# Performance work log

Hardware: AMD Instinct MI355X
Metric: run time of the kernel (lower is better)

Reference implementation:

```python
import jax, jax.numpy as jnp
import numpy as np

NUM_LEVELS = 16
LEVEL_DIM = 2
BASE_RES = 16
LOG2_HASH = 24
DESIRED_RES = 2048
D = 2
PRIMES = (1, 2654435761)
N_POINTS = 2097152
HIDDEN = 64
OUT_DIM = 3
LC_INIT = 1e-4


def _level_meta():
    # torch-ngp gridencoder level geometry (align_corners=False)
    S = np.log2(DESIRED_RES / BASE_RES) / (NUM_LEVELS - 1)
    max_params = 2 ** LOG2_HASH
    scales, res, offsets = [], [], [0]
    for l in range(NUM_LEVELS):
        s = 2.0 ** (l * S) * BASE_RES - 1.0
        r = int(np.ceil(s)) + 1
        p = min(max_params, (r + 1) ** D)
        p = int(np.ceil(p / 8) * 8)  # align to 8
        scales.append(s)
        res.append(r)
        offsets.append(offsets[-1] + p)
    return scales, res, offsets

SCALES, RES, OFFSETS = _level_meta()
TOTAL_PARAMS = OFFSETS[-1]  # 8827256 for this config


def hashgrid_encode(x01, embeddings):
    # x01: [N, 2] in [0,1]; embeddings: [TOTAL_PARAMS, LEVEL_DIM]
    feats = []
    for l in range(NUM_LEVELS):
        scale, r = SCALES[l], RES[l]
        size = OFFSETS[l + 1] - OFFSETS[l]
        dense = (r + 1) ** D <= size  # all levels dense for 2D / log2=24
        pos = x01 * jnp.float32(scale) + 0.5
        pg = jnp.floor(pos)
        frac = pos - pg  # [N,2] bilinear weights
        pgi = pg.astype(jnp.uint32)
        acc = jnp.zeros((x01.shape[0], LEVEL_DIM), x01.dtype)
        for cx in (0, 1):
            for cy in (0, 1):
                gx = pgi[:, 0] + jnp.uint32(cx)
                gy = pgi[:, 1] + jnp.uint32(cy)
                if dense:
                    idx = gx + gy * jnp.uint32(r + 1)
                else:
                    idx = (gx * jnp.uint32(PRIMES[0])) ^ (gy * jnp.uint32(PRIMES[1]))
                idx = (idx % jnp.uint32(size)).astype(jnp.int32) + OFFSETS[l]
                wx = frac[:, 0] if cx else 1.0 - frac[:, 0]
                wy = frac[:, 1] if cy else 1.0 - frac[:, 1]
                acc = acc + (wx * wy)[:, None] * embeddings[idx]
        feats.append(acc)
    return jnp.concatenate(feats, axis=-1)  # [N, 32]


def setup_inputs():
    key = jax.random.key(0)
    ks = jax.random.split(key, 5)
    in_feat = NUM_LEVELS * LEVEL_DIM  # 32

    def lin(k, fan_in, fan_out):
        b = 1.0 / np.sqrt(fan_in)
        kw, kb = jax.random.split(k)
        w = jax.random.uniform(kw, (fan_out, fan_in), jnp.float32, -b, b)
        bb = jax.random.uniform(kb, (fan_out,), jnp.float32, -b, b)
        return w, bb

    w0, b0 = lin(ks[1], in_feat, HIDDEN)
    w1, b1 = lin(ks[2], HIDDEN, HIDDEN)
    w2, b2 = lin(ks[3], HIDDEN, OUT_DIM)
    return {
        "x": jax.random.uniform(ks[0], (N_POINTS, 2), jnp.float32),
        "cmax": jnp.ones((2,), jnp.float32),
        "embeddings": jax.random.uniform(ks[4], (TOTAL_PARAMS, LEVEL_DIM), jnp.float32, -LC_INIT, LC_INIT),
        "w0": w0, "b0": b0, "w1": w1, "b1": b1, "w2": w2, "b2": b2,
    }


def reference(x, cmax, embeddings, w0, b0, w1, b1, w2, b2):
    x01 = x / cmax[::-1][None]  # cmax.flip(-1)
    out_lc0 = hashgrid_encode(x01, embeddings)
    h = jax.nn.relu(out_lc0)            # lc_act='relu'
    h = jax.nn.relu(h @ w0.T + b0)      # layer 0
    h = jax.nn.relu(h @ w1.T + b1)      # layer 1
    h = h @ w2.T + b2                   # layer 2 (no act)
    return h, out_lc0
```

## Files before the change

kernel.cpp:

```cpp
#include <hip/hip_runtime.h>
#include <math.h>

#define NLEV 16
#define RES  256
#define NBIN 65536

typedef _Float16 f16;
typedef f16 f16x8 __attribute__((ext_vector_type(8)));
typedef float f32x4 __attribute__((ext_vector_type(4)));

struct LevelMeta {
    float scale[NLEV];
    int   r1[NLEV];
    int   off[NLEV];
};

struct alignas(8) F4 { float x, y, z, w; };

__device__ inline unsigned spread2d(unsigned v) {
    v = (v | (v << 4)) & 0x0F0Fu;
    v = (v | (v << 2)) & 0x3333u;
    v = (v | (v << 1)) & 0x5555u;
    return v;
}

__device__ inline unsigned bin_of(float x0, float x1) {
    int bx = (int)(x0 * (float)RES); bx = bx < 0 ? 0 : (bx > RES - 1 ? RES - 1 : bx);
    int by = (int)(x1 * (float)RES); by = by < 0 ? 0 : (by > RES - 1 ? RES - 1 : by);
    return spread2d((unsigned)bx) | (spread2d((unsigned)by) << 1);
}

__global__ __launch_bounds__(256)
void zero_kernel(unsigned* __restrict__ hist) {
    ((uint4*)hist)[blockIdx.x * 256 + threadIdx.x] = uint4{0, 0, 0, 0};
}

__global__ __launch_bounds__(256)
void hist_kernel(const float* __restrict__ x, const float* __restrict__ cmax,
                 unsigned* __restrict__ hist, unsigned short* __restrict__ bin16,
                 unsigned* __restrict__ seq) {
    int p = blockIdx.x * 256 + threadIdx.x;
    float2 xy = ((const float2*)x)[p];
    unsigned b = bin_of(xy.x / cmax[1], xy.y / cmax[0]);
    unsigned s = atomicAdd(&hist[b], 1u);
    bin16[p] = (unsigned short)b;
    seq[p] = s;
}

__global__ __launch_bounds__(256)
void scanA_kernel(const unsigned* __restrict__ hist, unsigned* __restrict__ sums) {
    __shared__ unsigned ws[4];
    int t = threadIdx.x;
    unsigned s = hist[blockIdx.x * 256 + t];
#pragma unroll
    for (int o = 1; o < 64; o <<= 1) s += (unsigned)__shfl_xor((int)s, o);
    if ((t & 63) == 0) ws[t >> 6] = s;
    __syncthreads();
    if (t == 0) sums[blockIdx.x] = ws[0] + ws[1] + ws[2] + ws[3];
}

__global__ __launch_bounds__(256)
void scanB_kernel(unsigned* __restrict__ sums) {
    __shared__ unsigned ws[4];
    int t = threadIdx.x, lane = t & 63, w = t >> 6;
    unsigned v = sums[t];
    unsigned xs = v;
#pragma unroll
    for (int o = 1; o < 64; o <<= 1) {
        unsigned y = (unsigned)__shfl_up((int)xs, o);
        if (lane >= o) xs += y;
    }
    if (lane == 63) ws[w] = xs;
    __syncthreads();
    unsigned wo = 0;
    for (int k = 0; k < w; ++k) wo += ws[k];
    sums[t] = wo + xs - v;
}

__global__ __launch_bounds__(256)
void scanC_kernel(const unsigned* __restrict__ hist, const unsigned* __restrict__ sums,
                  unsigned* __restrict__ base) {
    __shared__ unsigned ws[4];
    int t = threadIdx.x, lane = t & 63, w = t >> 6;
    int gb = blockIdx.x * 256 + t;
    unsigned v = hist[gb];
    unsigned xs = v;
#pragma unroll
    for (int o = 1; o < 64; o <<= 1) {
        unsigned y = (unsigned)__shfl_up((int)xs, o);
        if (lane >= o) xs += y;
    }
    if (lane == 63) ws[w] = xs;
    __syncthreads();
    unsigned wo = 0;
    for (int k = 0; k < w; ++k) wo += ws[k];
    base[gb] = sums[blockIdx.x] + wo + xs - v;
}

__global__ __launch_bounds__(256)
void scatter_kernel(const float* __restrict__ x, const float* __restrict__ cmax,
                    const unsigned short* __restrict__ bin16,
                    const unsigned* __restrict__ seq,
                    const unsigned* __restrict__ base,
                    unsigned* __restrict__ pidx, float2* __restrict__ px) {
    int p = blockIdx.x * 256 + threadIdx.x;
    unsigned b = bin16[p];
    unsigned rank = base[b] + seq[p];
    pidx[rank] = (unsigned)p;
    float2 xy = ((const float2*)x)[p];
    float2 v; v.x = xy.x / cmax[1]; v.y = xy.y / cmax[0];
    px[rank] = v;
}

__global__ __launch_bounds__(256, 4)
void hashmlp_kernel(const float* __restrict__ x,
                    const float* __restrict__ cmax,
                    const unsigned* __restrict__ pidx,
                    const float2* __restrict__ px,
                    const float* __restrict__ emb,
                    const float* __restrict__ w0,
                    const float* __restrict__ b0,
                    const float* __restrict__ w1,
                    const float* __restrict__ b1,
                    const float* __restrict__ w2,
                    const float* __restrict__ b2,
                    float* __restrict__ out,
                    int npts, int nblk,
                    LevelMeta meta)
{
    __shared__ f16 wbuf[4][4608];

    const int tid  = threadIdx.x;
    const int lane = tid & 63;
    const int wave = tid >> 6;

    int bid = blockIdx.x;
    int cpx = nblk >> 3;
    int swz = (bid & 7) * cpx + (bid >> 3);
    const int g = swz * 256 + tid;
    const int gblk = swz * 256 + wave * 64;

    int p;
    float x0, x1;
    if (pidx) {
        p = (int)pidx[g];
        float2 xy = px[g];
        x0 = xy.x; x1 = xy.y;
    } else {
        p = g;
        float2 xy = ((const float2*)x)[p];
        x0 = xy.x / cmax[1];
        x1 = xy.y / cmax[0];
    }

    float fr[32];
#pragma unroll
    for (int hh = 0; hh < 2; ++hh) {
        F4 lo[8], hi[8];
#pragma unroll
        for (int i = 0; i < 8; ++i) {
            const int l = hh * 8 + i;
            float p0 = x0 * meta.scale[l] + 0.5f;
            float p1 = x1 * meta.scale[l] + 0.5f;
            int i0 = (int)floorf(p0);
            int i1 = (int)floorf(p1);
            const float* ebf = emb + 2 * (meta.off[l] + i1 * meta.r1[l] + i0);
            lo[i] = *(const F4*)ebf;
            hi[i] = *(const F4*)(ebf + 2 * meta.r1[l]);
        }
        __builtin_amdgcn_sched_barrier(0);
#pragma unroll
        for (int i = 0; i < 8; ++i) {
            const int l = hh * 8 + i;
            float p0 = x0 * meta.scale[l] + 0.5f;
            float p1 = x1 * meta.scale[l] + 0.5f;
            float g0 = floorf(p0), g1 = floorf(p1);
            float f0 = p0 - g0, f1 = p1 - g1;
            float omf0 = 1.f - f0, omf1 = 1.f - f1;
            float w00 = omf0 * omf1, w01 = omf0 * f1, w10 = f0 * omf1, w11 = f0 * f1;
            float a0 = w00 * lo[i].x; a0 += w01 * hi[i].x; a0 += w10 * lo[i].z; a0 += w11 * hi[i].z;
            float a1 = w00 * lo[i].y; a1 += w01 * hi[i].y; a1 += w10 * lo[i].w; a1 += w11 * hi[i].w;
            fr[2 * l]     = a0;
            fr[2 * l + 1] = a1;
        }
    }

    float* outlc = out + (size_t)npts * 3 + (size_t)p * 32;
#pragma unroll
    for (int c = 0; c < 8; ++c) {
        float4 v;
        v.x = fr[4 * c]; v.y = fr[4 * c + 1]; v.z = fr[4 * c + 2]; v.w = fr[4 * c + 3];
        ((float4*)outlc)[c] = v;
    }

    f16* fbuf = wbuf[wave];
#pragma unroll
    for (int c = 0; c < 4; ++c) {
        f16x8 v;
#pragma unroll
        for (int j = 0; j < 8; ++j)
            v[j] = (f16)(fmaxf(fr[8 * c + j], 0.f) * 16384.f);
        *(f16x8*)&fbuf[lane * 40 + c * 8] = v;
    }

    const int lr = lane & 15;
    const int lg = lane >> 4;
    f16* hbuf = wbuf[wave];

    {
        f16x8 bf[4];
        float bia[4];
#pragma unroll
        for (int nt = 0; nt < 4; ++nt) {
            const float* wr = w0 + (nt * 16 + lr) * 32 + lg * 8;
            float4 wa = ((const float4*)wr)[0];
            float4 wb = ((const float4*)wr)[1];
            f16x8 v;
            v[0] = (f16)wa.x; v[1] = (f16)wa.y; v[2] = (f16)wa.z; v[3] = (f16)wa.w;
            v[4] = (f16)wb.x; v[5] = (f16)wb.y; v[6] = (f16)wb.z; v[7] = (f16)wb.w;
            bf[nt] = v;
            bia[nt] = b0[nt * 16 + lr];
        }
#pragma unroll
        for (int mt = 3; mt >= 0; --mt) {
            f16x8 a = *(const f16x8*)&fbuf[(mt * 16 + lr) * 40 + lg * 8];
            __builtin_amdgcn_s_setprio(1);
            f32x4 c[4];
#pragma unroll
            for (int nt = 0; nt < 4; ++nt) {
                f32x4 z = {0.f, 0.f, 0.f, 0.f};
                c[nt] = __builtin_amdgcn_mfma_f32_16x16x32_f16(a, bf[nt], z, 0, 0, 0);
            }
            __builtin_amdgcn_s_setprio(0);
#pragma unroll
            for (int nt = 0; nt < 4; ++nt)
#pragma unroll
                for (int q = 0; q < 4; ++q) {
                    float h = fmaxf(c[nt][q] * (1.0f / 16384.f) + bia[nt], 0.f);
                    hbuf[(mt * 16 + lg * 4 + q) * 72 + nt * 16 + lr] = (f16)h;
                }
        }
    }

    {
        f16x8 bf[4][2];
        float bia[4];
#pragma unroll
        for (int nt = 0; nt < 4; ++nt) {
            const float* wr = w1 + (nt * 16 + lr) * 64;
#pragma unroll
            for (int h = 0; h < 2; ++h) {
                float4 wa = ((const float4*)(wr + 32 * h + lg * 8))[0];
                float4 wb = ((const float4*)(wr + 32 * h + lg * 8))[1];
                f16x8 v;
                v[0] = (f16)wa.x; v[1] = (f16)wa.y; v[2] = (f16)wa.z; v[3] = (f16)wa.w;
                v[4] = (f16)wb.x; v[5] = (f16)wb.y; v[6] = (f16)wb.z; v[7] = (f16)wb.w;
                bf[nt][h] = v;
            }
            bia[nt] = b1[nt * 16 + lr];
        }
#pragma unroll
        for (int mt = 0; mt < 4; ++mt) {
            f16x8 a0 = *(const f16x8*)&hbuf[(mt * 16 + lr) * 72 + lg * 8];
            f16x8 a1 = *(const f16x8*)&hbuf[(mt * 16 + lr) * 72 + 32 + lg * 8];
            __builtin_amdgcn_s_setprio(1);
            f32x4 c[4];
#pragma unroll
            for (int nt = 0; nt < 4; ++nt) {
                f32x4 z = {0.f, 0.f, 0.f, 0.f};
                z = __builtin_amdgcn_mfma_f32_16x16x32_f16(a0, bf[nt][0], z, 0, 0, 0);
                c[nt] = __builtin_amdgcn_mfma_f32_16x16x32_f16(a1, bf[nt][1], z, 0, 0, 0);
            }
            __builtin_amdgcn_s_setprio(0);
#pragma unroll
            for (int nt = 0; nt < 4; ++nt)
#pragma unroll
                for (int q = 0; q < 4; ++q) {
                    float h = fmaxf(c[nt][q] + bia[nt], 0.f);
                    hbuf[(mt * 16 + lg * 4 + q) * 72 + nt * 16 + lr] = (f16)h;
                }
        }
    }

    {
        f16x8 bf0 = {};
        f16x8 bf1 = {};
        float bia2 = 0.f;
        if (lr < 3) {
            const float* wr = w2 + lr * 64;
#pragma unroll
            for (int h = 0; h < 2; ++h) {
                float4 wa = ((const float4*)(wr + 32 * h + lg * 8))[0];
                float4 wb = ((const float4*)(wr + 32 * h + lg * 8))[1];
                f16x8 v;
                v[0] = (f16)wa.x; v[1] = (f16)wa.y; v[2] = (f16)wa.z; v[3] = (f16)wa.w;
                v[4] = (f16)wb.x; v[5] = (f16)wb.y; v[6] = (f16)wb.z; v[7] = (f16)wb.w;
                if (h) bf1 = v; else bf0 = v;
            }
            bia2 = b2[lr];
        }
#pragma unroll
        for (int mt = 0; mt < 4; ++mt) {
            f16x8 a0 = *(const f16x8*)&hbuf[(mt * 16 + lr) * 72 + lg * 8];
            f16x8 a1 = *(const f16x8*)&hbuf[(mt * 16 + lr) * 72 + 32 + lg * 8];
            __builtin_amdgcn_s_setprio(1);
            f32x4 c = {0.f, 0.f, 0.f, 0.f};
            c = __builtin_amdgcn_mfma_f32_16x16x32_f16(a0, bf0, c, 0, 0, 0);
            c = __builtin_amdgcn_mfma_f32_16x16x32_f16(a1, bf1, c, 0, 0, 0);
            __builtin_amdgcn_s_setprio(0);
            if (lr < 3) {
#pragma unroll
                for (int q = 0; q < 4; ++q) {
                    int row = mt * 16 + lg * 4 + q;
                    int po = pidx ? (int)pidx[gblk + row] : (gblk + row);
                    out[(size_t)po * 3 + lr] = c[q] + bia2;
                }
            }
        }
    }
}

extern "C" void kernel_launch(void* const* d_in, const int* in_sizes, int n_in,
                              void* d_out, int out_size, void* d_ws, size_t ws_size,
                              hipStream_t stream) {
    const float* x    = (const float*)d_in[0];
    const float* cmax = (const float*)d_in[1];
    const float* emb  = (const float*)d_in[2];
    const float* w0   = (const float*)d_in[3];
    const float* b0   = (const float*)d_in[4];
    const float* w1   = (const float*)d_in[5];
    const float* b1   = (const float*)d_in[6];
    const float* w2   = (const float*)d_in[7];
    const float* b2   = (const float*)d_in[8];
    const int npts = in_sizes[0] / 2;
    const int nblk = npts / 256;

    LevelMeta meta;
    const double S = log2(2048.0 / 16.0) / 15.0;
    long long off = 0;
    for (int l = 0; l < NLEV; ++l) {
        double s = pow(2.0, l * S) * 16.0 - 1.0;
        int r = (int)ceil(s) + 1;
        long long pc = (long long)(r + 1) * (r + 1);
        if (pc > (1ll << 24)) pc = (1ll << 24);
        pc = ((pc + 7) / 8) * 8;
        meta.scale[l] = (float)s;
        meta.r1[l]    = r + 1;
        meta.off[l]   = (int)off;
        off += pc;
    }

    size_t need = (size_t)NBIN * 8 + 256 * 4 + (size_t)npts * 18;
    if (ws_size >= need && (npts & 255) == 0 && (nblk & 7) == 0) {
        unsigned* hist = (unsigned*)d_ws;
        unsigned* base = hist + NBIN;
        unsigned* sums = base + NBIN;
        unsigned* pidx = sums + 256;
        unsigned* seq  = pidx + npts;
        float2*   px   = (float2*)(seq + npts);
        unsigned short* bin16 = (unsigned short*)(px + npts);

        hipLaunchKernelGGL(zero_kernel, dim3(NBIN / 1024), dim3(256), 0, stream, hist);
        hipLaunchKernelGGL(hist_kernel, dim3(nblk), dim3(256), 0, stream, x, cmax, hist, bin16, seq);
        hipLaunchKernelGGL(scanA_kernel, dim3(NBIN / 256), dim3(256), 0, stream, hist, sums);
        hipLaunchKernelGGL(scanB_kernel, dim3(1), dim3(256), 0, stream, sums);
        hipLaunchKernelGGL(scanC_kernel, dim3(NBIN / 256), dim3(256), 0, stream, hist, sums, base);
        hipLaunchKernelGGL(scatter_kernel, dim3(nblk), dim3(256), 0, stream, x, cmax, bin16, seq, base, pidx, px);
        hipLaunchKernelGGL(hashmlp_kernel, dim3(nblk), dim3(256), 0, stream,
                           x, cmax, pidx, px, emb, w0, b0, w1, b1, w2, b2,
                           (float*)d_out, npts, nblk, meta);
    } else {
        hipLaunchKernelGGL(hashmlp_kernel, dim3(nblk), dim3(256), 0, stream,
                           x, cmax, (const unsigned*)nullptr, (const float2*)nullptr,
                           emb, w0, b0, w1, b1, w2, b2,
                           (float*)d_out, npts, nblk, meta);
    }
}
```

Measured before the change: 402.2 us.

## Split fused hash-encode+MLP kernel into separate encode and MLP kernels

The fused kernel is split into an encode kernel that gathers embeddings (using inline-asm dwordx4 loads followed by an explicit vmcnt wait) and writes the 32-float features, and a separate MLP kernel that reads those features back in original point order. The MLP now runs on contiguous points, which removes the pidx indirection and scattered output writes, and each kernel needs fewer registers and less LDS. The cost is an extra launch plus a full re-read of the 256 MB feature buffer from memory.

```diff
diff --git a/kernel.cpp b/kernel.cpp
--- a/kernel.cpp
+++ b/kernel.cpp
@@ -15,7 +15,12 @@
     int   off[NLEV];
 };
 
-struct alignas(8) F4 { float x, y, z, w; };
+__device__ inline f32x4 gload4(const float* p) {
+    f32x4 r;
+    asm volatile("global_load_dwordx4 %0, %1, off"
+                 : "=v"(r) : "v"(p) : "memory");
+    return r;
+}
 
 __device__ inline unsigned spread2d(unsigned v) {
     v = (v | (v << 4)) & 0x0F0Fu;
@@ -113,32 +118,19 @@
 }
 
 __global__ __launch_bounds__(256, 4)
-void hashmlp_kernel(const float* __restrict__ x,
-                    const float* __restrict__ cmax,
-                    const unsigned* __restrict__ pidx,
-                    const float2* __restrict__ px,
-                    const float* __restrict__ emb,
-                    const float* __restrict__ w0,
-                    const float* __restrict__ b0,
-                    const float* __restrict__ w1,
-                    const float* __restrict__ b1,
-                    const float* __restrict__ w2,
-                    const float* __restrict__ b2,
-                    float* __restrict__ out,
-                    int npts, int nblk,
-                    LevelMeta meta)
+void encode_kernel(const float* __restrict__ x,
+                   const float* __restrict__ cmax,
+                   const unsigned* __restrict__ pidx,
+                   const float2* __restrict__ px,
+                   const float* __restrict__ emb,
+                   float* __restrict__ out,
+                   int npts, int nblk,
+                   LevelMeta meta)
 {
-    __shared__ f16 wbuf[4][4608];
-
-    const int tid  = threadIdx.x;
-    const int lane = tid & 63;
-    const int wave = tid >> 6;
-
     int bid = blockIdx.x;
     int cpx = nblk >> 3;
     int swz = (bid & 7) * cpx + (bid >> 3);
-    const int g = swz * 256 + tid;
-    const int gblk = swz * 256 + wave * 64;
+    const int g = swz * 256 + threadIdx.x;
 
     int p;
     float x0, x1;
@@ -153,10 +145,11 @@
         x1 = xy.y / cmax[0];
     }
 
-    float fr[32];
+    float* outlc = out + (size_t)npts * 3 + (size_t)p * 32;
+
 #pragma unroll
     for (int hh = 0; hh < 2; ++hh) {
-        F4 lo[8], hi[8];
+        f32x4 lo[8], hi[8];
 #pragma unroll
         for (int i = 0; i < 8; ++i) {
             const int l = hh * 8 + i;
@@ -165,10 +158,13 @@
             int i0 = (int)floorf(p0);
             int i1 = (int)floorf(p1);
             const float* ebf = emb + 2 * (meta.off[l] + i1 * meta.r1[l] + i0);
-            lo[i] = *(const F4*)ebf;
-            hi[i] = *(const F4*)(ebf + 2 * meta.r1[l]);
-        }
+            lo[i] = gload4(ebf);
+            hi[i] = gload4(ebf + 2 * meta.r1[l]);
+        }
+        asm volatile("s_waitcnt vmcnt(0)" ::: "memory");
         __builtin_amdgcn_sched_barrier(0);
+
+        float fr[16];
 #pragma unroll
         for (int i = 0; i < 8; ++i) {
             const int l = hh * 8 + i;
@@ -178,34 +174,59 @@
             float f0 = p0 - g0, f1 = p1 - g1;
             float omf0 = 1.f - f0, omf1 = 1.f - f1;
             float w00 = omf0 * omf1, w01 = omf0 * f1, w10 = f0 * omf1, w11 = f0 * f1;
-            float a0 = w00 * lo[i].x; a0 += w01 * hi[i].x; a0 += w10 * lo[i].z; a0 += w11 * hi[i].z;
-            float a1 = w00 * lo[i].y; a1 += w01 * hi[i].y; a1 += w10 * lo[i].w; a1 += w11 * hi[i].w;
-            fr[2 * l]     = a0;
-            fr[2 * l + 1] = a1;
-        }
-    }
-
-    float* outlc = out + (size_t)npts * 3 + (size_t)p * 32;
-#pragma unroll
-    for (int c = 0; c < 8; ++c) {
-        float4 v;
-        v.x = fr[4 * c]; v.y = fr[4 * c + 1]; v.z = fr[4 * c + 2]; v.w = fr[4 * c + 3];
-        ((float4*)outlc)[c] = v;
-    }
-
-    f16* fbuf = wbuf[wave];
-#pragma unroll
-    for (int c = 0; c < 4; ++c) {
-        f16x8 v;
-#pragma unroll
-        for (int j = 0; j < 8; ++j)
-            v[j] = (f16)(fmaxf(fr[8 * c + j], 0.f) * 16384.f);
-        *(f16x8*)&fbuf[lane * 40 + c * 8] = v;
-    }
+            float a0 = w00 * lo[i][0]; a0 += w01 * hi[i][0]; a0 += w10 * lo[i][2]; a0 += w11 * hi[i][2];
+            float a1 = w00 * lo[i][1]; a1 += w01 * hi[i][1]; a1 += w10 * lo[i][3]; a1 += w11 * hi[i][3];
+            fr[2 * i]     = a0;
+            fr[2 * i + 1] = a1;
+        }
+#pragma unroll
+        for (int c = 0; c < 4; ++c) {
+            float4 v;
+            v.x = fr[4 * c]; v.y = fr[4 * c + 1]; v.z = fr[4 * c + 2]; v.w = fr[4 * c + 3];
+            ((float4*)outlc)[hh * 4 + c] = v;
+        }
+    }
+}
+
+__global__ __launch_bounds__(256, 4)
+void mlp_kernel(const float* __restrict__ lc,
+                const float* __restrict__ w0,
+                const float* __restrict__ b0,
+                const float* __restrict__ w1,
+                const float* __restrict__ b1,
+                const float* __restrict__ w2,
+                const float* __restrict__ b2,
+                float* __restrict__ out,
+                int npts)
+{
+    __shared__ f16 wbuf[4][4608];
+
+    const int tid  = threadIdx.x;
+    const int lane = tid & 63;
+    const int wave = tid >> 6;
+    const int g0 = blockIdx.x * 256 + wave * 64;
 
     const int lr = lane & 15;
     const int lg = lane >> 4;
     f16* hbuf = wbuf[wave];
+
+    f16x8 afr[4];
+#pragma unroll
+    for (int mt = 0; mt < 4; ++mt) {
+        const float* fp = lc + (size_t)(g0 + mt * 16 + lr) * 32 + lg * 8;
+        float4 fa = ((const float4*)fp)[0];
+        float4 fb = ((const float4*)fp)[1];
+        f16x8 v;
+        v[0] = (f16)(fmaxf(fa.x, 0.f) * 16384.f);
+        v[1] = (f16)(fmaxf(fa.y, 0.f) * 16384.f);
+        v[2] = (f16)(fmaxf(fa.z, 0.f) * 16384.f);
+        v[3] = (f16)(fmaxf(fa.w, 0.f) * 16384.f);
+        v[4] = (f16)(fmaxf(fb.x, 0.f) * 16384.f);
+        v[5] = (f16)(fmaxf(fb.y, 0.f) * 16384.f);
+        v[6] = (f16)(fmaxf(fb.z, 0.f) * 16384.f);
+        v[7] = (f16)(fmaxf(fb.w, 0.f) * 16384.f);
+        afr[mt] = v;
+    }
 
     {
         f16x8 bf[4];
@@ -222,14 +243,13 @@
             bia[nt] = b0[nt * 16 + lr];
         }
 #pragma unroll
-        for (int mt = 3; mt >= 0; --mt) {
-            f16x8 a = *(const f16x8*)&fbuf[(mt * 16 + lr) * 40 + lg * 8];
+        for (int mt = 0; mt < 4; ++mt) {
             __builtin_amdgcn_s_setprio(1);
             f32x4 c[4];
 #pragma unroll
             for (int nt = 0; nt < 4; ++nt) {
                 f32x4 z = {0.f, 0.f, 0.f, 0.f};
-                c[nt] = __builtin_amdgcn_mfma_f32_16x16x32_f16(a, bf[nt], z, 0, 0, 0);
+                c[nt] = __builtin_amdgcn_mfma_f32_16x16x32_f16(afr[mt], bf[nt], z, 0, 0, 0);
             }
             __builtin_amdgcn_s_setprio(0);
 #pragma unroll
@@ -312,8 +332,7 @@
 #pragma unroll
                 for (int q = 0; q < 4; ++q) {
                     int row = mt * 16 + lg * 4 + q;
-                    int po = pidx ? (int)pidx[gblk + row] : (gblk + row);
-                    out[(size_t)po * 3 + lr] = c[q] + bia2;
+                    out[(size_t)(g0 + row) * 3 + lr] = c[q] + bia2;
                 }
             }
         }
@@ -350,6 +369,9 @@
         off += pc;
     }
 
+    float* outp = (float*)d_out;
+    const float* lc = outp + (size_t)npts * 3;
+
     size_t need = (size_t)NBIN * 8 + 256 * 4 + (size_t)npts * 18;
     if (ws_size >= need && (npts & 255) == 0 && (nblk & 7) == 0) {
         unsigned* hist = (unsigned*)d_ws;
@@ -366,13 +388,13 @@
         hipLaunchKernelGGL(scanB_kernel, dim3(1), dim3(256), 0, stream, sums);
         hipLaunchKernelGGL(scanC_kernel, dim3(NBIN / 256), dim3(256), 0, stream, hist, sums, base);
         hipLaunchKernelGGL(scatter_kernel, dim3(nblk), dim3(256), 0, stream, x, cmax, bin16, seq, base, pidx, px);
-        hipLaunchKernelGGL(hashmlp_kernel, dim3(nblk), dim3(256), 0, stream,
-                           x, cmax, pidx, px, emb, w0, b0, w1, b1, w2, b2,
-                           (float*)d_out, npts, nblk, meta);
+        hipLaunchKernelGGL(encode_kernel, dim3(nblk), dim3(256), 0, stream,
+                           x, cmax, pidx, px, emb, outp, npts, nblk, meta);
     } else {
-        hipLaunchKernelGGL(hashmlp_kernel, dim3(nblk), dim3(256), 0, stream,
+        hipLaunchKernelGGL(encode_kernel, dim3(nblk), dim3(256), 0, stream,
                            x, cmax, (const unsigned*)nullptr, (const float2*)nullptr,
-                           emb, w0, b0, w1, b1, w2, b2,
-                           (float*)d_out, npts, nblk, meta);
-    }
-}
+                           emb, outp, npts, nblk, meta);
+    }
+    hipLaunchKernelGGL(mlp_kernel, dim3(nblk), dim3(256), 0, stream,
+                       lc, w0, b0, w1, b1, w2, b2, outp, npts);
+}
```

Result: slower. 459.8 us (+14.3%).
